# Performance work log

Hardware: AMD Instinct MI355X
Metric: run time of the kernel (lower is better)

## Reference

```python
import jax, jax.numpy as jnp
import numpy as np

B, L, IDIM = 1, 1024, 2048
H, DK, DV, K = 16, 128, 128, 4
KEY_DIM = H * DK          # 2048
VAL_DIM = H * DV          # 2048
CONV_DIM = 2 * KEY_DIM + VAL_DIM  # 6144
EPS = 1e-6


def setup_inputs() -> dict:
    key = jax.random.key(0)
    ks = jax.random.split(key, 8)
    s = 0.02
    x = jax.random.normal(ks[0], (B, L, IDIM), jnp.float32)
    Wqkv = jax.random.normal(ks[1], (IDIM, CONV_DIM), jnp.float32) * s
    Wz = jax.random.normal(ks[2], (IDIM, VAL_DIM), jnp.float32) * s
    Wb = jax.random.normal(ks[3], (IDIM, H), jnp.float32) * s
    Wa = jax.random.normal(ks[4], (IDIM, H), jnp.float32) * s
    conv_w = jax.random.normal(ks[5], (CONV_DIM, 1, K), jnp.float32) * 0.2  # depthwise [O,I/g=1,K]
    A_log = jnp.log(jax.random.uniform(ks[6], (H,), jnp.float32, 0.1, 16.0))
    dt_bias = jnp.ones((H,), jnp.float32)
    norm_w = jnp.ones((DV,), jnp.float32)
    Wout = jax.random.normal(ks[7], (VAL_DIM, IDIM), jnp.float32) * s
    return dict(x=x, Wqkv=Wqkv, Wz=Wz, Wb=Wb, Wa=Wa, conv_w=conv_w,
                A_log=A_log, dt_bias=dt_bias, norm_w=norm_w, Wout=Wout)


def _l2norm(t):
    return t * jax.lax.rsqrt(jnp.sum(t * t, axis=-1, keepdims=True) + EPS)


def reference(x, Wqkv, Wz, Wb, Wa, conv_w, A_log, dt_bias, norm_w, Wout):
    b, l, _ = x.shape
    # fused QKV projection + causal depthwise conv + SiLU
    qkv = jnp.einsum('bld,dc->blc', x, Wqkv)                 # [B,L,CONV_DIM]
    qkv = jnp.transpose(qkv, (0, 2, 1))                      # [B,C,L]
    qkv = jax.lax.conv_general_dilated(
        qkv, conv_w, window_strides=(1,), padding=[(K - 1, 0)],
        dimension_numbers=('NCL', 'OIL', 'NCL'), feature_group_count=CONV_DIM)
    qkv = jax.nn.silu(jnp.transpose(qkv, (0, 2, 1)))         # [B,L,C]
    q, k, v = jnp.split(qkv, [KEY_DIM, 2 * KEY_DIM], axis=-1)

    z = jnp.einsum('bld,dv->blv', x, Wz)                     # [B,L,VAL_DIM]
    beta = jax.nn.sigmoid(jnp.einsum('bld,dh->blh', x, Wb))  # [B,L,H]
    A = -jnp.exp(A_log)                                      # [H]
    dt = jax.nn.softplus(jnp.einsum('bld,dh->blh', x, Wa) + dt_bias)
    g = dt * A                                               # [B,L,H] (negative)

    q = _l2norm(q.reshape(b, l, H, DK))
    k = _l2norm(k.reshape(b, l, H, DK))
    v = v.reshape(b, l, H, DV)
    scale = DK ** -0.5

    # time-major for scan: [L,B,H,...]
    qs = jnp.transpose(q, (1, 0, 2, 3)) * scale
    ks_ = jnp.transpose(k, (1, 0, 2, 3))
    vs = jnp.transpose(v, (1, 0, 2, 3))
    bs = jnp.transpose(beta, (1, 0, 2))
    gs = jnp.transpose(g, (1, 0, 2))

    M0 = jnp.zeros((b, H, DK, DV), jnp.float32)

    def step(M, inp):
        q_t, k_t, v_t, b_t, g_t = inp
        M = M * jnp.exp(g_t)[..., None, None]                    # decay
        Mk = jnp.einsum('bhd,bhdv->bhv', k_t, M)                 # readout of old mem
        M = M + jnp.einsum('bhd,bhv->bhdv', k_t, (v_t - Mk) * b_t[..., None])
        o_t = jnp.einsum('bhd,bhdv->bhv', q_t, M)
        return M, o_t

    _, out = jax.lax.scan(step, M0, (qs, ks_, vs, bs, gs))   # out: [L,B,H,DV]
    out = jnp.transpose(out, (1, 0, 2, 3))                   # [B,L,H,DV]

    # RMSNormGated: rms_norm(o) * weight * silu(z)
    zg = z.reshape(b, l, H, DV)
    rms = jax.lax.rsqrt(jnp.mean(out * out, axis=-1, keepdims=True) + EPS)
    out = (out * rms) * norm_w * jax.nn.silu(zg)

    out = out.reshape(b, l, VAL_DIM)
    return jnp.einsum('blv,vd->bld', out, Wout)
```

## Files before the change

### kernel.cpp

```cpp
#include <hip/hip_runtime.h>

typedef short bf16x8 __attribute__((ext_vector_type(8)));
typedef float f32x4 __attribute__((ext_vector_type(4)));
typedef float f32x2 __attribute__((ext_vector_type(2)));
typedef unsigned short u16;
typedef u16 u16x4 __attribute__((ext_vector_type(4)));

#define L_SEQ 1024
#define IDIM_ 2048
#define H_ 16
#define DK_ 128
#define DV_ 128
#define KEYD 2048
#define VALD 2048
#define CONVD 6144
#define QZD 8320
#define GCOL 8192
#define SCH 64
#define NSC (L_SEQ / SCH)

__device__ __forceinline__ u16 f2bf(float f) {
  union { float f; unsigned u; } v; v.f = f;
  unsigned r = v.u + 0x7FFF + ((v.u >> 16) & 1);
  return (u16)(r >> 16);
}

__device__ __forceinline__ float red16(float x) {
  union U { float f; int i; } a, t;
  a.f = x;
  t.i = __builtin_amdgcn_update_dpp(0, a.i, 0xB1, 0xF, 0xF, true); a.f += t.f;
  t.i = __builtin_amdgcn_update_dpp(0, a.i, 0x4E, 0xF, 0xF, true); a.f += t.f;
  t.i = __builtin_amdgcn_update_dpp(0, a.i, 0x141, 0xF, 0xF, true); a.f += t.f;
  t.i = __builtin_amdgcn_update_dpp(0, a.i, 0x140, 0xF, 0xF, true); a.f += t.f;
  return a.f;
}

__global__ __launch_bounds__(256) void prepcast_kernel(const float* __restrict__ x,
                                                       const float* __restrict__ Wqkv,
                                                       const float* __restrict__ Wz,
                                                       const float* __restrict__ Wb,
                                                       const float* __restrict__ Wa,
                                                       const float* __restrict__ Wout,
                                                       u16* __restrict__ xb,
                                                       u16* __restrict__ WcatT,
                                                       u16* __restrict__ WoutT) {
  __shared__ float tile[32][33];
  const int bid = blockIdx.x;
  if (bid < 2048) {
    int i = (bid * 256 + threadIdx.x) * 4;
    f32x4 v = *(const f32x4*)&x[i];
    u16x4 o = { f2bf(v[0]), f2bf(v[1]), f2bf(v[2]), f2bf(v[3]) };
    *(u16x4*)&xb[i] = o;
    return;
  }
  if (bid >= 22592) {
    size_t off = (size_t)8224 * IDIM_ + (size_t)(bid - 22592) * 8192 + threadIdx.x * 32;
    u16x4 z = {0, 0, 0, 0};
#pragma unroll
    for (int j = 0; j < 8; ++j) *(u16x4*)&WcatT[off + j * 4] = z;
    return;
  }
  if (bid >= 22528) {
    int by = bid - 22528;
    int r = threadIdx.x >> 3, c8 = threadIdx.x & 7;
    int row = by * 32 + r;
#pragma unroll
    for (int cc = 0; cc < 2; ++cc) {
      int c = cc * 8 + c8;
      WcatT[(size_t)(GCOL + c) * IDIM_ + row]      = f2bf(Wb[(size_t)row * 16 + c]);
      WcatT[(size_t)(GCOL + 16 + c) * IDIM_ + row] = f2bf(Wa[(size_t)row * 16 + c]);
    }
    return;
  }
  const float* W; u16* WT; int R, C, bx, by;
  if (bid < 14336) {
    int t = bid - 2048;  bx = t % 192; by = t / 192;
    W = Wqkv; WT = WcatT; R = IDIM_; C = CONVD;
  } else if (bid < 18432) {
    int t = bid - 14336; bx = t & 63; by = t >> 6;
    W = Wz; WT = WcatT + (size_t)CONVD * IDIM_; R = IDIM_; C = VALD;
  } else {
    int t = bid - 18432; bx = t & 63; by = t >> 6;
    W = Wout; WT = WoutT; R = VALD; C = IDIM_;
  }
  int c0 = bx * 32, r0 = by * 32;
  int tx = threadIdx.x & 31, ty = threadIdx.x >> 5;
#pragma unroll
  for (int j = 0; j < 4; ++j)
    tile[ty + j * 8][tx] = W[(size_t)(r0 + ty + j * 8) * C + c0 + tx];
  __syncthreads();
#pragma unroll
  for (int j = 0; j < 4; ++j)
    WT[(size_t)(c0 + ty + j * 8) * R + r0 + tx] = f2bf(tile[tx][ty + j * 8]);
}

__global__ __launch_bounds__(256) void gemm_bt_kernel(const u16* __restrict__ A,
                                                      const u16* __restrict__ B,
                                                      float* __restrict__ C,
                                                      int M, int N, int K) {
  __shared__ short As[128 * 72];
  __shared__ short Bs[128 * 72];
  const int tid = threadIdx.x;
  const int lane = tid & 63, wave = tid >> 6;
  const int wm = wave >> 1, wn = wave & 1;
  const int m0 = blockIdx.y * 128, n0 = blockIdx.x * 128;
  const int l15 = lane & 15, lhi = lane >> 4;

  f32x4 acc[4][4] = {};

  for (int k0 = 0; k0 < K; k0 += 64) {
    __syncthreads();
#pragma unroll
    for (int i = 0; i < 4; ++i) {
      int chunk = tid + i * 256;
      int row = chunk >> 3;
      int kc = (chunk & 7) * 8;
      *(bf16x8*)&As[row * 72 + kc] =
          *(const bf16x8*)&A[(size_t)(m0 + row) * K + k0 + kc];
      *(bf16x8*)&Bs[row * 72 + kc] =
          *(const bf16x8*)&B[(size_t)(n0 + row) * K + k0 + kc];
    }
    __syncthreads();
#pragma unroll
    for (int kk = 0; kk < 64; kk += 32) {
      const int koff = kk + lhi * 8;
      bf16x8 a[4], b[4];
#pragma unroll
      for (int m = 0; m < 4; ++m)
        a[m] = *(const bf16x8*)&As[(wm * 64 + m * 16 + l15) * 72 + koff];
#pragma unroll
      for (int n = 0; n < 4; ++n)
        b[n] = *(const bf16x8*)&Bs[(wn * 64 + n * 16 + l15) * 72 + koff];
#pragma unroll
      for (int m = 0; m < 4; ++m)
#pragma unroll
        for (int n = 0; n < 4; ++n)
          acc[m][n] = __builtin_amdgcn_mfma_f32_16x16x32_bf16(a[m], b[n], acc[m][n], 0, 0, 0);
    }
  }
#pragma unroll
  for (int m = 0; m < 4; ++m)
#pragma unroll
    for (int n = 0; n < 4; ++n)
#pragma unroll
      for (int j = 0; j < 4; ++j) {
        int row = m0 + wm * 64 + m * 16 + lhi * 4 + j;
        int col = n0 + wn * 64 + n * 16 + l15;
        C[(size_t)row * N + col] = acc[m][n][j];
      }
}

__global__ __launch_bounds__(256) void gemm_bt64_kernel(const u16* __restrict__ A,
                                                        const u16* __restrict__ B,
                                                        float* __restrict__ C,
                                                        int M, int N, int K, int cxl) {
  __shared__ short As[64 * 72];
  __shared__ short Bs[128 * 72];
  const int tid = threadIdx.x;
  const int lane = tid & 63, wave = tid >> 6;
  const int wm = wave >> 1, wn = wave & 1;
  const int bid = blockIdx.x;
  const int xcd = bid & 7, bi = bid >> 3;
  const int bx = (xcd << cxl) + (bi & ((1 << cxl) - 1));
  const int by = bi >> cxl;
  const int m0 = by * 64, n0 = bx * 128;
  const int l15 = lane & 15, lhi = lane >> 4;

  f32x4 acc[2][4] = {};

  for (int k0 = 0; k0 < K; k0 += 64) {
    __syncthreads();
#pragma unroll
    for (int i = 0; i < 2; ++i) {
      int chunk = tid + i * 256;
      int row = chunk >> 3;
      int kc = (chunk & 7) * 8;
      *(bf16x8*)&As[row * 72 + kc] =
          *(const bf16x8*)&A[(size_t)(m0 + row) * K + k0 + kc];
    }
#pragma unroll
    for (int i = 0; i < 4; ++i) {
      int chunk = tid + i * 256;
      int row = chunk >> 3;
      int kc = (chunk & 7) * 8;
      *(bf16x8*)&Bs[row * 72 + kc] =
          *(const bf16x8*)&B[(size_t)(n0 + row) * K + k0 + kc];
    }
    __syncthreads();
#pragma unroll
    for (int kk = 0; kk < 64; kk += 32) {
      const int koff = kk + lhi * 8;
      bf16x8 a[2], b[4];
#pragma unroll
      for (int m = 0; m < 2; ++m)
        a[m] = *(const bf16x8*)&As[(wm * 32 + m * 16 + l15) * 72 + koff];
#pragma unroll
      for (int n = 0; n < 4; ++n)
        b[n] = *(const bf16x8*)&Bs[(wn * 64 + n * 16 + l15) * 72 + koff];
#pragma unroll
      for (int m = 0; m < 2; ++m)
#pragma unroll
        for (int n = 0; n < 4; ++n)
          acc[m][n] = __builtin_amdgcn_mfma_f32_16x16x32_bf16(a[m], b[n], acc[m][n], 0, 0, 0);
    }
  }
#pragma unroll
  for (int m = 0; m < 2; ++m)
#pragma unroll
    for (int n = 0; n < 4; ++n)
#pragma unroll
      for (int j = 0; j < 4; ++j) {
        int row = m0 + wm * 32 + m * 16 + lhi * 4 + j;
        int col = n0 + wn * 64 + n * 16 + l15;
        C[(size_t)row * N + col] = acc[m][n][j];
      }
}

__global__ __launch_bounds__(256) void gatelite_kernel(const float* __restrict__ qkvz,
                                                       const float* __restrict__ A_log,
                                                       const float* __restrict__ dt_bias,
                                                       float* __restrict__ btT,
                                                       float* __restrict__ gT) {
  int gid = blockIdx.x * 256 + threadIdx.x;
  int l = gid >> 4, h = gid & 15;
  const float* row = qkvz + (size_t)l * QZD + GCOL;
  float b = row[h], a = row[16 + h];
  btT[h * L_SEQ + l] = 1.f / (1.f + expf(-b));
  float dtv = a + dt_bias[h];
  dtv = (dtv > 20.f) ? dtv : log1pf(expf(dtv));
  gT[h * L_SEQ + l] = -expf(A_log[h]) * dtv;
}

__global__ __launch_bounds__(256) void prep2_kernel(const float* __restrict__ qkvz,
                                                    const float* __restrict__ cw,
                                                    float* __restrict__ qn,
                                                    float* __restrict__ kn,
                                                    float* __restrict__ vT) {
  __shared__ float tile[32][33];
  const int bid = blockIdx.x;
  if (bid < 4096) {
    int wid = bid * 4 + (threadIdx.x >> 6);
    int lane = threadIdx.x & 63;
    int l = wid >> 4, h = wid & 15;
    const int cq = h * 128 + lane * 2;
    const int ck = KEYD + cq;
    const float* row0 = qkvz + (size_t)l * QZD;
    f32x4 wq0 = *(const f32x4*)&cw[cq * 4];
    f32x4 wq1 = *(const f32x4*)&cw[(cq + 1) * 4];
    f32x4 wk0 = *(const f32x4*)&cw[ck * 4];
    f32x4 wk1 = *(const f32x4*)&cw[(ck + 1) * 4];
    f32x2 xq = *(const f32x2*)&row0[cq];
    f32x2 xk = *(const f32x2*)&row0[ck];
    float q0 = xq[0] * wq0[3], q1 = xq[1] * wq1[3];
    float k0 = xk[0] * wk0[3], k1 = xk[1] * wk1[3];
    if (l >= 1) {
      f32x2 aq = *(const f32x2*)&row0[cq - QZD];
      f32x2 ak = *(const f32x2*)&row0[ck - QZD];
      q0 += aq[0] * wq0[2]; q1 += aq[1] * wq1[2];
      k0 += ak[0] * wk0[2]; k1 += ak[1] * wk1[2];
    }
    if (l >= 2) {
      f32x2 aq = *(const f32x2*)&row0[cq - 2 * QZD];
      f32x2 ak = *(const f32x2*)&row0[ck - 2 * QZD];
      q0 += aq[0] * wq0[1]; q1 += aq[1] * wq1[1];
      k0 += ak[0] * wk0[1]; k1 += ak[1] * wk1[1];
    }
    if (l >= 3) {
      f32x2 aq = *(const f32x2*)&row0[cq - 3 * QZD];
      f32x2 ak = *(const f32x2*)&row0[ck - 3 * QZD];
      q0 += aq[0] * wq0[0]; q1 += aq[1] * wq1[0];
      k0 += ak[0] * wk0[0]; k1 += ak[1] * wk1[0];
    }
    f32x2 qv = { q0 / (1.f + expf(-q0)), q1 / (1.f + expf(-q1)) };
    f32x2 kv = { k0 / (1.f + expf(-k0)), k1 / (1.f + expf(-k1)) };

    float ssq = qv[0] * qv[0] + qv[1] * qv[1];
    float ssk = kv[0] * kv[0] + kv[1] * kv[1];
#pragma unroll
    for (int s = 1; s < 64; s <<= 1) {
      ssq += __shfl_xor(ssq, s);
      ssk += __shfl_xor(ssk, s);
    }
    float scq = 0.08838834764831845f / sqrtf(ssq + 1e-6f);
    float sck = 1.f / sqrtf(ssk + 1e-6f);
    qv[0] *= scq; qv[1] *= scq;
    kv[0] *= sck; kv[1] *= sck;
    size_t base = ((size_t)h * L_SEQ + l) * 128 + lane * 2;
    *(f32x2*)&qn[base] = qv;
    *(f32x2*)&kn[base] = kv;
    return;
  }
  int t = bid - 4096;
  int c0 = (t & 63) * 32, l0 = (t >> 6) * 32;
  int tx = threadIdx.x & 31, ty = threadIdx.x >> 5;
  const int c = 2 * KEYD + c0 + tx;
  f32x4 w = *(const f32x4*)&cw[c * 4];
#pragma unroll
  for (int j = 0; j < 4; ++j) {
    int l = l0 + ty + j * 8;
    const float* p = qkvz + (size_t)l * QZD + c;
    float s = p[0] * w[3];
    if (l >= 1) s += p[-QZD] * w[2];
    if (l >= 2) s += p[-2 * QZD] * w[1];
    if (l >= 3) s += p[-3 * QZD] * w[0];
    tile[ty + j * 8][tx] = s / (1.f + expf(-s));
  }
  __syncthreads();
#pragma unroll
  for (int j = 0; j < 4; ++j)
    vT[(size_t)(c0 + ty + j * 8) * L_SEQ + l0 + tx] = tile[tx][ty + j * 8];
}

__global__ __launch_bounds__(256) void winv_kernel(const float* __restrict__ kn,
                                                   const float* __restrict__ gT,
                                                   const float* __restrict__ btT,
                                                   float* __restrict__ Wg) {
  __shared__ alignas(16) u16 kb[64][136];
  __shared__ float Nl[64][65];
  __shared__ float gsh[64], Gh[64], bts[64];

  const int tid = threadIdx.x;
  const int lane = tid & 63, wave = tid >> 6;
  const int l15 = lane & 15, lhi = lane >> 4;
  const int h = blockIdx.x & 15, sc = blockIdx.x >> 4;
  const int l0 = sc * SCH;

  {
    int t = tid >> 2, c0 = (tid & 3) * 32;
    const float* kr = kn + ((size_t)h * L_SEQ + l0 + t) * 128 + c0;
#pragma unroll
    for (int j = 0; j < 8; ++j) {
      f32x4 vk = *(const f32x4*)&kr[j * 4];
      u16x4 ok = { f2bf(vk[0]), f2bf(vk[1]), f2bf(vk[2]), f2bf(vk[3]) };
      *(u16x4*)&kb[t][c0 + j * 4] = ok;
    }
  }
  if (tid < 64) {
    gsh[tid] = gT[h * L_SEQ + l0 + tid];
    bts[tid] = btT[h * L_SEQ + l0 + tid];
  }
  __syncthreads();
  if (tid < 64) {
    float a = 0.f;
    for (int u = 0; u <= tid; ++u) a += gsh[u];
    Gh[tid] = a;
  }
  __syncthreads();

  f32x4 acc1[2][2] = {};
  const int wm = wave >> 1, wn = wave & 1;
#pragma unroll
  for (int kk = 0; kk < 128; kk += 32) {
    const int koff = kk + lhi * 8;
    bf16x8 a[2], b[2];
#pragma unroll
    for (int m = 0; m < 2; ++m)
      a[m] = *(const bf16x8*)&kb[wm * 32 + m * 16 + l15][koff];
#pragma unroll
    for (int n = 0; n < 2; ++n)
      b[n] = *(const bf16x8*)&kb[wn * 32 + n * 16 + l15][koff];
#pragma unroll
    for (int m = 0; m < 2; ++m)
#pragma unroll
      for (int n = 0; n < 2; ++n)
        acc1[m][n] = __builtin_amdgcn_mfma_f32_16x16x32_bf16(a[m], b[n], acc1[m][n], 0, 0, 0);
  }
#pragma unroll
  for (int m = 0; m < 2; ++m)
#pragma unroll
    for (int n = 0; n < 2; ++n)
#pragma unroll
      for (int j = 0; j < 4; ++j) {
        int t = wm * 32 + m * 16 + lhi * 4 + j;
        int s = wn * 32 + n * 16 + l15;
        Nl[t][s] = (s < t) ? bts[t] * expf(Gh[t] - Gh[s]) * acc1[m][n][j] : 0.f;
      }
  __syncthreads();

  if (wave == 0) {
    float w[64];
    w[0] = (lane == 0) ? 1.f : 0.f;
#pragma unroll
    for (int t = 1; t < 64; ++t) {
      float a0 = (lane == t) ? 1.f : 0.f, a1 = 0.f;
#pragma unroll
      for (int s = 0; s + 1 < t; s += 2) {
        a0 = fmaf(-Nl[t][s], w[s], a0);
        a1 = fmaf(-Nl[t][s + 1], w[s + 1], a1);
      }
      if (t & 1) a0 = fmaf(-Nl[t][t - 1], w[t - 1], a0);
      w[t] = a0 + a1;
    }
    size_t base = (size_t)(sc * 16 + h) * 4096 + (size_t)lane * 64;
#pragma unroll
    for (int s = 0; s < 64; ++s) Wg[base + s] = w[s];
  }
}

__global__ __launch_bounds__(256) void wyscan_kernel(const float* __restrict__ kn,
                                                     const float* __restrict__ vT,
                                                     const float* __restrict__ gT,
                                                     const float* __restrict__ btT,
                                                     const float* __restrict__ Wg,
                                                     float* __restrict__ Mb,
                                                     float* __restrict__ DbT) {
  __shared__ alignas(16) u16 kb[64][136];
  __shared__ alignas(16) u16 kbT[128][72];
  __shared__ alignas(16) u16 Wbf[64][72];
  __shared__ alignas(16) u16 rTb[128][72];
  __shared__ alignas(16) u16 ddT[128][72];
  __shared__ alignas(16) u16 MbfT[128][136];
  __shared__ float gsh[64], Gh[64], bts[64];

  const int tid = threadIdx.x;
  const int lane = tid & 63, wave = tid >> 6;
  const int l15 = lane & 15, lhi = lane >> 4;
  const int wm = wave >> 1, wn = wave & 1;
  const int h = blockIdx.x;

  for (int i = tid; i < 128 * 136; i += 256) (&MbfT[0][0])[i] = 0;
  f32x4 Mreg[4][4];
#pragma unroll
  for (int m = 0; m < 4; ++m)
#pragma unroll
    for (int n = 0; n < 4; ++n) Mreg[m][n] = (f32x4){0.f, 0.f, 0.f, 0.f};
  __syncthreads();

#pragma unroll 1
  for (int c = 0; c < NSC; ++c) {
    const int l0 = c * SCH;
#pragma unroll
    for (int m = 0; m < 4; ++m)
#pragma unroll
      for (int n = 0; n < 4; ++n) {
        int dv = wn * 64 + n * 16 + l15;
        int dk0 = wm * 64 + m * 16 + lhi * 4;
        *(f32x4*)&Mb[(((size_t)(c * 16 + h)) * 128 + dv) * 128 + dk0] = Mreg[m][n];
      }
    {
      int t = tid >> 2, c0 = (tid & 3) * 32;
      const float* kr = kn + ((size_t)h * L_SEQ + l0 + t) * 128 + c0;
#pragma unroll
      for (int j = 0; j < 32; ++j) {
        u16 kv = f2bf(kr[j]);
        kb[t][c0 + j] = kv;
        kbT[c0 + j][t] = kv;
      }
    }
    {
      int t = tid >> 2, s0 = (tid & 3) * 16;
      size_t base = (size_t)(c * 16 + h) * 4096;
#pragma unroll
      for (int i = 0; i < 16; ++i)
        Wbf[t][s0 + i] = f2bf(Wg[base + (size_t)(s0 + i) * 64 + t]);
    }
    if (tid < 64) {
      gsh[tid] = gT[h * L_SEQ + l0 + tid];
      bts[tid] = btT[h * L_SEQ + l0 + tid];
    }
    __syncthreads();
    if (tid < 64) {
      float a = 0.f;
      for (int u = 0; u <= tid; ++u) a += gsh[u];
      Gh[tid] = a;
    }
    __syncthreads();

    {
      f32x4 acc[2][4] = {};
#pragma unroll
      for (int kk = 0; kk < 128; kk += 32) {
        const int koff = kk + lhi * 8;
        bf16x8 a[2], b[4];
#pragma unroll
        for (int m = 0; m < 2; ++m)
          a[m] = *(const bf16x8*)&kb[wm * 32 + m * 16 + l15][koff];
#pragma unroll
        for (int n = 0; n < 4; ++n)
          b[n] = *(const bf16x8*)&MbfT[wn * 64 + n * 16 + l15][koff];
#pragma unroll
        for (int m = 0; m < 2; ++m)
#pragma unroll
          for (int n = 0; n < 4; ++n)
            acc[m][n] = __builtin_amdgcn_mfma_f32_16x16x32_bf16(a[m], b[n], acc[m][n], 0, 0, 0);
      }
#pragma unroll
      for (int m = 0; m < 2; ++m)
#pragma unroll
        for (int n = 0; n < 4; ++n) {
          int dv = wn * 64 + n * 16 + l15;
          int t0 = wm * 32 + m * 16 + lhi * 4;
          f32x4 v4 = *(const f32x4*)&vT[(size_t)(h * 128 + dv) * L_SEQ + l0 + t0];
#pragma unroll
          for (int j = 0; j < 4; ++j) {
            int t = t0 + j;
            float r = bts[t] * (v4[j] - expf(Gh[t]) * acc[m][n][j]);
            rTb[dv][t] = f2bf(r);
          }
        }
    }
    __syncthreads();

    {
      f32x4 acc[2][4] = {};
#pragma unroll
      for (int kk = 0; kk < 64; kk += 32) {
        const int koff = kk + lhi * 8;
        bf16x8 a[2], b[4];
#pragma unroll
        for (int m = 0; m < 2; ++m)
          a[m] = *(const bf16x8*)&Wbf[wm * 32 + m * 16 + l15][koff];
#pragma unroll
        for (int n = 0; n < 4; ++n)
          b[n] = *(const bf16x8*)&rTb[wn * 64 + n * 16 + l15][koff];
#pragma unroll
        for (int m = 0; m < 2; ++m)
#pragma unroll
          for (int n = 0; n < 4; ++n)
            acc[m][n] = __builtin_amdgcn_mfma_f32_16x16x32_bf16(a[m], b[n], acc[m][n], 0, 0, 0);
      }
      const float G63 = Gh[63];
#pragma unroll
      for (int m = 0; m < 2; ++m)
#pragma unroll
        for (int n = 0; n < 4; ++n) {
          int dv = wn * 64 + n * 16 + l15;
          int t0 = wm * 32 + m * 16 + lhi * 4;
          *(f32x4*)&DbT[(size_t)(h * 128 + dv) * L_SEQ + l0 + t0] = acc[m][n];
#pragma unroll
          for (int j = 0; j < 4; ++j) {
            int t = t0 + j;
            ddT[dv][t] = f2bf(acc[m][n][j] * expf(G63 - Gh[t]));
          }
        }
    }
    __syncthreads();

    {
      const float E63 = expf(Gh[63]);
      f32x4 acc[4][4];
#pragma unroll
      for (int m = 0; m < 4; ++m)
#pragma unroll
        for (int n = 0; n < 4; ++n)
#pragma unroll
          for (int j = 0; j < 4; ++j) acc[m][n][j] = E63 * Mreg[m][n][j];
#pragma unroll
      for (int kk = 0; kk < 64; kk += 32) {
        const int koff = kk + lhi * 8;
        bf16x8 a[4], b[4];
#pragma unroll
        for (int m = 0; m < 4; ++m)
          a[m] = *(const bf16x8*)&kbT[wm * 64 + m * 16 + l15][koff];
#pragma unroll
        for (int n = 0; n < 4; ++n)
          b[n] = *(const bf16x8*)&ddT[wn * 64 + n * 16 + l15][koff];
#pragma unroll
        for (int m = 0; m < 4; ++m)
#pragma unroll
          for (int n = 0; n < 4; ++n)
            acc[m][n] = __builtin_amdgcn_mfma_f32_16x16x32_bf16(a[m], b[n], acc[m][n], 0, 0, 0);
      }
#pragma unroll
      for (int m = 0; m < 4; ++m)
#pragma unroll
        for (int n = 0; n < 4; ++n) {
          Mreg[m][n] = acc[m][n];
          int dv = wn * 64 + n * 16 + l15;
          int dk0 = wm * 64 + m * 16 + lhi * 4;
#pragma unroll
          for (int j = 0; j < 4; ++j)
            MbfT[dv][dk0 + j] = f2bf(acc[m][n][j]);
        }
    }
    __syncthreads();
  }
}

__global__ __launch_bounds__(256) void opass_kernel(const float* __restrict__ qn,
                                                    const float* __restrict__ kn,
                                                    const float* __restrict__ DbT,
                                                    const float* __restrict__ gT,
                                                    const float* __restrict__ Mb,
                                                    const float* __restrict__ qkvz,
                                                    const float* __restrict__ norm_w,
                                                    u16* __restrict__ gn) {
  __shared__ alignas(16) u16 qsb[64][136];
  __shared__ alignas(16) u16 bbuf[128][136];
  __shared__ alignas(16) u16 Asb[64][72];
  __shared__ float gsh[64], Gh[64];
  __shared__ float ssr[2][64];

  const int tid = threadIdx.x;
  const int lane = tid & 63, wave = tid >> 6;
  const int l15 = lane & 15, lhi = lane >> 4;
  const int h = blockIdx.x & 15, sc = blockIdx.x >> 4;
  const int l0 = sc * SCH;

  {
    int t = tid >> 2, c0 = (tid & 3) * 32;
    const float* qr = qn + ((size_t)h * L_SEQ + l0 + t) * 128 + c0;
    const float* kr = kn + ((size_t)h * L_SEQ + l0 + t) * 128 + c0;
#pragma unroll
    for (int j = 0; j < 8; ++j) {
      f32x4 vq = *(const f32x4*)&qr[j * 4];
      f32x4 vk = *(const f32x4*)&kr[j * 4];
      u16x4 oq = { f2bf(vq[0]), f2bf(vq[1]), f2bf(vq[2]), f2bf(vq[3]) };
      u16x4 ok = { f2bf(vk[0]), f2bf(vk[1]), f2bf(vk[2]), f2bf(vk[3]) };
      *(u16x4*)&qsb[t][c0 + j * 4] = oq;
      *(u16x4*)&bbuf[t][c0 + j * 4] = ok;
    }
  }
  if (tid < 64) gsh[tid] = gT[h * L_SEQ + l0 + tid];
  __syncthreads();
  if (tid < 64) {
    float a = 0.f;
    for (int u = 0; u <= tid; ++u) a += gsh[u];
    Gh[tid] = a;
  }
  __syncthreads();

  f32x4 acc1[2][2] = {};
  const int wm = wave >> 1, wn = wave & 1;
#pragma unroll
  for (int kk = 0; kk < 128; kk += 32) {
    const int koff = kk + lhi * 8;
    bf16x8 a[2], b[2];
#pragma unroll
    for (int m = 0; m < 2; ++m)
      a[m] = *(const bf16x8*)&qsb[wm * 32 + m * 16 + l15][koff];
#pragma unroll
    for (int n = 0; n < 2; ++n)
      b[n] = *(const bf16x8*)&bbuf[wn * 32 + n * 16 + l15][koff];
#pragma unroll
    for (int m = 0; m < 2; ++m)
#pragma unroll
      for (int n = 0; n < 2; ++n)
        acc1[m][n] = __builtin_amdgcn_mfma_f32_16x16x32_bf16(a[m], b[n], acc1[m][n], 0, 0, 0);
  }
#pragma unroll
  for (int m = 0; m < 2; ++m)
#pragma unroll
    for (int n = 0; n < 2; ++n)
#pragma unroll
      for (int j = 0; j < 4; ++j) {
        int t = wm * 32 + m * 16 + lhi * 4 + j;
        int s = wn * 32 + n * 16 + l15;
        float a = (s <= t) ? acc1[m][n][j] * expf(Gh[t] - Gh[s]) : 0.f;
        Asb[t][s] = f2bf(a);
      }
  __syncthreads();

  {
    int dv = tid >> 1, c0 = (tid & 1) * 64;
    const float* mr = Mb + (((size_t)sc * 16 + h) * 128 + dv) * 128 + c0;
#pragma unroll
    for (int j = 0; j < 16; ++j) {
      f32x4 v = *(const f32x4*)&mr[j * 4];
      u16x4 o = { f2bf(v[0]), f2bf(v[1]), f2bf(v[2]), f2bf(v[3]) };
      *(u16x4*)&bbuf[dv][c0 + j * 4] = o;
    }
  }
  __syncthreads();

  f32x4 acc[2][4] = {};
#pragma unroll
  for (int kk = 0; kk < 128; kk += 32) {
    const int koff = kk + lhi * 8;
    bf16x8 a[2], b[4];
#pragma unroll
    for (int m = 0; m < 2; ++m)
      a[m] = *(const bf16x8*)&qsb[wm * 32 + m * 16 + l15][koff];
#pragma unroll
    for (int n = 0; n < 4; ++n)
      b[n] = *(const bf16x8*)&bbuf[wn * 64 + n * 16 + l15][koff];
#pragma unroll
    for (int m = 0; m < 2; ++m)
#pragma unroll
      for (int n = 0; n < 4; ++n)
        acc[m][n] = __builtin_amdgcn_mfma_f32_16x16x32_bf16(a[m], b[n], acc[m][n], 0, 0, 0);
  }
#pragma unroll
  for (int m = 0; m < 2; ++m) {
#pragma unroll
    for (int j = 0; j < 4; ++j) {
      int t = wm * 32 + m * 16 + lhi * 4 + j;
      float sc1 = expf(Gh[t]);
#pragma unroll
      for (int n = 0; n < 4; ++n) acc[m][n][j] *= sc1;
    }
  }
  __syncthreads();

  {
    int dv = tid >> 1, c0 = (tid & 1) * 32;
    const float* dr = DbT + (size_t)(h * 128 + dv) * L_SEQ + l0 + c0;
#pragma unroll
    for (int j = 0; j < 8; ++j) {
      f32x4 v = *(const f32x4*)&dr[j * 4];
      u16x4 o = { f2bf(v[0]), f2bf(v[1]), f2bf(v[2]), f2bf(v[3]) };
      *(u16x4*)&bbuf[dv][c0 + j * 4] = o;
    }
  }
  __syncthreads();

#pragma unroll
  for (int kk = 0; kk < 64; kk += 32) {
    const int koff = kk + lhi * 8;
    bf16x8 a[2], b[4];
#pragma unroll
    for (int m = 0; m < 2; ++m)
      a[m] = *(const bf16x8*)&Asb[wm * 32 + m * 16 + l15][koff];
#pragma unroll
    for (int n = 0; n < 4; ++n)
      b[n] = *(const bf16x8*)&bbuf[wn * 64 + n * 16 + l15][koff];
#pragma unroll
    for (int m = 0; m < 2; ++m)
#pragma unroll
      for (int n = 0; n < 4; ++n)
        acc[m][n] = __builtin_amdgcn_mfma_f32_16x16x32_bf16(a[m], b[n], acc[m][n], 0, 0, 0);
  }

  float pr[2][4];
#pragma unroll
  for (int m = 0; m < 2; ++m)
#pragma unroll
    for (int j = 0; j < 4; ++j) {
      float p = 0.f;
#pragma unroll
      for (int n = 0; n < 4; ++n) p = fmaf(acc[m][n][j], acc[m][n][j], p);
      pr[m][j] = red16(p);
    }
  if (l15 == 0) {
#pragma unroll
    for (int m = 0; m < 2; ++m)
#pragma unroll
      for (int j = 0; j < 4; ++j)
        ssr[wn][wm * 32 + m * 16 + lhi * 4 + j] = pr[m][j];
  }
  __syncthreads();
#pragma unroll
  for (int m = 0; m < 2; ++m)
#pragma unroll
    for (int j = 0; j < 4; ++j) {
      int t = wm * 32 + m * 16 + lhi * 4 + j;
      float ss = ssr[0][t] + ssr[1][t];
      float r = 1.f / sqrtf(ss * (1.f / 128.f) + 1e-6f);
      const float* zp = qkvz + (size_t)(l0 + t) * QZD + CONVD + h * 128;
      u16* dst = gn + (size_t)(l0 + t) * VALD + h * 128;
#pragma unroll
      for (int n = 0; n < 4; ++n) {
        int dv = wn * 64 + n * 16 + l15;
        float z = zp[dv];
        float sil = z / (1.f + expf(-z));
        dst[dv] = f2bf(acc[m][n][j] * r * norm_w[dv] * sil);
      }
    }
}

extern "C" void kernel_launch(void* const* d_in, const int* in_sizes, int n_in,
                              void* d_out, int out_size, void* d_ws, size_t ws_size,
                              hipStream_t stream) {
  const float* x      = (const float*)d_in[0];
  const float* Wqkv   = (const float*)d_in[1];
  const float* Wz     = (const float*)d_in[2];
  const float* Wb     = (const float*)d_in[3];
  const float* Wa     = (const float*)d_in[4];
  const float* conv_w = (const float*)d_in[5];
  const float* A_log  = (const float*)d_in[6];
  const float* dt_bias= (const float*)d_in[7];
  const float* norm_w = (const float*)d_in[8];
  const float* Wout   = (const float*)d_in[9];
  float* out = (float*)d_out;

  char* ws = (char*)d_ws;
  size_t off = 0;
  auto alloc = [&](size_t bytes) {
    void* p = ws + off;
    off = (off + bytes + 255) & ~(size_t)255;
    return p;
  };
  u16* xb     = (u16*)alloc((size_t)L_SEQ * IDIM_ * 2);
  u16* WcatT  = (u16*)alloc((size_t)QZD * IDIM_ * 2);
  u16* WoutT  = (u16*)alloc((size_t)IDIM_ * VALD * 2);
  float* qkvz = (float*)alloc((size_t)L_SEQ * QZD * 4);
  float* qn   = (float*)alloc((size_t)H_ * L_SEQ * 128 * 4);
  float* kn   = (float*)alloc((size_t)H_ * L_SEQ * 128 * 4);
  float* vT   = (float*)alloc((size_t)H_ * 128 * L_SEQ * 4);
  float* btT  = (float*)alloc((size_t)L_SEQ * H_ * 4);
  float* gTb  = (float*)alloc((size_t)L_SEQ * H_ * 4);
  float* Wgb  = (float*)alloc((size_t)NSC * H_ * 64 * 64 * 4);
  float* Mb   = (float*)alloc((size_t)NSC * H_ * 128 * 128 * 4);
  float* DbT  = (float*)alloc((size_t)H_ * 128 * L_SEQ * 4);
  u16* gn     = (u16*)alloc((size_t)L_SEQ * VALD * 2);

  prepcast_kernel<<<22616, 256, 0, stream>>>(x, Wqkv, Wz, Wb, Wa, Wout, xb, WcatT, WoutT);

  gemm_bt_kernel<<<dim3(QZD / 128, L_SEQ / 128), 256, 0, stream>>>(xb, WcatT, qkvz, L_SEQ, QZD, IDIM_);

  gatelite_kernel<<<64, 256, 0, stream>>>(qkvz, A_log, dt_bias, btT, gTb);

  prep2_kernel<<<6144, 256, 0, stream>>>(qkvz, conv_w, qn, kn, vT);

  winv_kernel<<<NSC * H_, 256, 0, stream>>>(kn, gTb, btT, Wgb);
  wyscan_kernel<<<H_, 256, 0, stream>>>(kn, vT, gTb, btT, Wgb, Mb, DbT);

  opass_kernel<<<NSC * H_, 256, 0, stream>>>(qn, kn, DbT, gTb, Mb, qkvz, norm_w, gn);

  gemm_bt64_kernel<<<256, 256, 0, stream>>>(gn, WoutT, out, L_SEQ, IDIM_, VALD, 1);
}
```

Before: 362.8 us.

## Split wyscan state across DV slabs to launch four blocks per head

The sequential chunked state-update kernel now splits the 128-wide value dimension into four 32-wide slabs, so it launches 64 blocks instead of 16. Each block carries a quarter of the state matrix in registers and shared memory, which shortens the serial per-chunk chain and uses more compute units. In exchange every slab block redundantly loads and converts the key chunk and W matrix. The global loads of k and W are also vectorised to float4, and a barrier is added after the state store.

```diff
diff --git a/kernel.cpp b/kernel.cpp
--- a/kernel.cpp
+++ b/kernel.cpp
@@ -407,52 +407,61 @@
   __shared__ alignas(16) u16 kb[64][136];
   __shared__ alignas(16) u16 kbT[128][72];
   __shared__ alignas(16) u16 Wbf[64][72];
-  __shared__ alignas(16) u16 rTb[128][72];
-  __shared__ alignas(16) u16 ddT[128][72];
-  __shared__ alignas(16) u16 MbfT[128][136];
+  __shared__ alignas(16) u16 rTb[32][72];
+  __shared__ alignas(16) u16 ddT[32][72];
+  __shared__ alignas(16) u16 MbfT[32][136];
   __shared__ float gsh[64], Gh[64], bts[64];
 
   const int tid = threadIdx.x;
   const int lane = tid & 63, wave = tid >> 6;
   const int l15 = lane & 15, lhi = lane >> 4;
   const int wm = wave >> 1, wn = wave & 1;
-  const int h = blockIdx.x;
-
-  for (int i = tid; i < 128 * 136; i += 256) (&MbfT[0][0])[i] = 0;
-  f32x4 Mreg[4][4];
-#pragma unroll
-  for (int m = 0; m < 4; ++m)
-#pragma unroll
-    for (int n = 0; n < 4; ++n) Mreg[m][n] = (f32x4){0.f, 0.f, 0.f, 0.f};
+  const int h = blockIdx.x & 15, slab = blockIdx.x >> 4;
+  const int dv0 = slab * 32;
+  const int dvl = wn * 16 + l15;
+
+  for (int i = tid; i < 32 * 136; i += 256) (&MbfT[0][0])[i] = 0;
+  f32x4 Mreg[4];
+#pragma unroll
+  for (int m = 0; m < 4; ++m) Mreg[m] = (f32x4){0.f, 0.f, 0.f, 0.f};
   __syncthreads();
 
 #pragma unroll 1
   for (int c = 0; c < NSC; ++c) {
     const int l0 = c * SCH;
 #pragma unroll
-    for (int m = 0; m < 4; ++m)
-#pragma unroll
-      for (int n = 0; n < 4; ++n) {
-        int dv = wn * 64 + n * 16 + l15;
-        int dk0 = wm * 64 + m * 16 + lhi * 4;
-        *(f32x4*)&Mb[(((size_t)(c * 16 + h)) * 128 + dv) * 128 + dk0] = Mreg[m][n];
-      }
+    for (int m = 0; m < 4; ++m) {
+      int dk0 = wm * 64 + m * 16 + lhi * 4;
+      *(f32x4*)&Mb[(((size_t)(c * 16 + h)) * 128 + dv0 + dvl) * 128 + dk0] = Mreg[m];
+    }
+    __syncthreads();
+
     {
       int t = tid >> 2, c0 = (tid & 3) * 32;
       const float* kr = kn + ((size_t)h * L_SEQ + l0 + t) * 128 + c0;
 #pragma unroll
-      for (int j = 0; j < 32; ++j) {
-        u16 kv = f2bf(kr[j]);
-        kb[t][c0 + j] = kv;
-        kbT[c0 + j][t] = kv;
+      for (int j4 = 0; j4 < 8; ++j4) {
+        f32x4 v = *(const f32x4*)&kr[j4 * 4];
+        u16x4 o = { f2bf(v[0]), f2bf(v[1]), f2bf(v[2]), f2bf(v[3]) };
+        *(u16x4*)&kb[t][c0 + j4 * 4] = o;
+        kbT[c0 + j4 * 4 + 0][t] = o[0];
+        kbT[c0 + j4 * 4 + 1][t] = o[1];
+        kbT[c0 + j4 * 4 + 2][t] = o[2];
+        kbT[c0 + j4 * 4 + 3][t] = o[3];
       }
     }
     {
-      int t = tid >> 2, s0 = (tid & 3) * 16;
       size_t base = (size_t)(c * 16 + h) * 4096;
 #pragma unroll
-      for (int i = 0; i < 16; ++i)
-        Wbf[t][s0 + i] = f2bf(Wg[base + (size_t)(s0 + i) * 64 + t]);
+      for (int i = 0; i < 4; ++i) {
+        int flat = tid + i * 256;
+        int s = flat >> 4, t0 = (flat & 15) * 4;
+        f32x4 v = *(const f32x4*)&Wg[base + (size_t)s * 64 + t0];
+        Wbf[t0 + 0][s] = f2bf(v[0]);
+        Wbf[t0 + 1][s] = f2bf(v[1]);
+        Wbf[t0 + 2][s] = f2bf(v[2]);
+        Wbf[t0 + 3][s] = f2bf(v[3]);
+      }
     }
     if (tid < 64) {
       gsh[tid] = gT[h * L_SEQ + l0 + tid];
@@ -467,111 +476,82 @@
     __syncthreads();
 
     {
-      f32x4 acc[2][4] = {};
+      f32x4 acc[2] = {};
 #pragma unroll
       for (int kk = 0; kk < 128; kk += 32) {
         const int koff = kk + lhi * 8;
-        bf16x8 a[2], b[4];
-#pragma unroll
-        for (int m = 0; m < 2; ++m)
-          a[m] = *(const bf16x8*)&kb[wm * 32 + m * 16 + l15][koff];
-#pragma unroll
-        for (int n = 0; n < 4; ++n)
-          b[n] = *(const bf16x8*)&MbfT[wn * 64 + n * 16 + l15][koff];
-#pragma unroll
-        for (int m = 0; m < 2; ++m)
-#pragma unroll
-          for (int n = 0; n < 4; ++n)
-            acc[m][n] = __builtin_amdgcn_mfma_f32_16x16x32_bf16(a[m], b[n], acc[m][n], 0, 0, 0);
-      }
-#pragma unroll
-      for (int m = 0; m < 2; ++m)
-#pragma unroll
-        for (int n = 0; n < 4; ++n) {
-          int dv = wn * 64 + n * 16 + l15;
-          int t0 = wm * 32 + m * 16 + lhi * 4;
-          f32x4 v4 = *(const f32x4*)&vT[(size_t)(h * 128 + dv) * L_SEQ + l0 + t0];
-#pragma unroll
-          for (int j = 0; j < 4; ++j) {
-            int t = t0 + j;
-            float r = bts[t] * (v4[j] - expf(Gh[t]) * acc[m][n][j]);
-            rTb[dv][t] = f2bf(r);
-          }
+        bf16x8 b0 = *(const bf16x8*)&MbfT[dvl][koff];
+#pragma unroll
+        for (int m = 0; m < 2; ++m) {
+          bf16x8 a = *(const bf16x8*)&kb[wm * 32 + m * 16 + l15][koff];
+          acc[m] = __builtin_amdgcn_mfma_f32_16x16x32_bf16(a, b0, acc[m], 0, 0, 0);
         }
+      }
+#pragma unroll
+      for (int m = 0; m < 2; ++m) {
+        int t0 = wm * 32 + m * 16 + lhi * 4;
+        f32x4 v4 = *(const f32x4*)&vT[(size_t)(h * 128 + dv0 + dvl) * L_SEQ + l0 + t0];
+#pragma unroll
+        for (int j = 0; j < 4; ++j) {
+          int t = t0 + j;
+          float r = bts[t] * (v4[j] - expf(Gh[t]) * acc[m][j]);
+          rTb[dvl][t] = f2bf(r);
+        }
+      }
     }
     __syncthreads();
 
     {
-      f32x4 acc[2][4] = {};
+      f32x4 acc[2] = {};
 #pragma unroll
       for (int kk = 0; kk < 64; kk += 32) {
         const int koff = kk + lhi * 8;
-        bf16x8 a[2], b[4];
-#pragma unroll
-        for (int m = 0; m < 2; ++m)
-          a[m] = *(const bf16x8*)&Wbf[wm * 32 + m * 16 + l15][koff];
-#pragma unroll
-        for (int n = 0; n < 4; ++n)
-          b[n] = *(const bf16x8*)&rTb[wn * 64 + n * 16 + l15][koff];
-#pragma unroll
-        for (int m = 0; m < 2; ++m)
-#pragma unroll
-          for (int n = 0; n < 4; ++n)
-            acc[m][n] = __builtin_amdgcn_mfma_f32_16x16x32_bf16(a[m], b[n], acc[m][n], 0, 0, 0);
+        bf16x8 b0 = *(const bf16x8*)&rTb[dvl][koff];
+#pragma unroll
+        for (int m = 0; m < 2; ++m) {
+          bf16x8 a = *(const bf16x8*)&Wbf[wm * 32 + m * 16 + l15][koff];
+          acc[m] = __builtin_amdgcn_mfma_f32_16x16x32_bf16(a, b0, acc[m], 0, 0, 0);
+        }
       }
       const float G63 = Gh[63];
 #pragma unroll
-      for (int m = 0; m < 2; ++m)
-#pragma unroll
-        for (int n = 0; n < 4; ++n) {
-          int dv = wn * 64 + n * 16 + l15;
-          int t0 = wm * 32 + m * 16 + lhi * 4;
-          *(f32x4*)&DbT[(size_t)(h * 128 + dv) * L_SEQ + l0 + t0] = acc[m][n];
-#pragma unroll
-          for (int j = 0; j < 4; ++j) {
-            int t = t0 + j;
-            ddT[dv][t] = f2bf(acc[m][n][j] * expf(G63 - Gh[t]));
-          }
+      for (int m = 0; m < 2; ++m) {
+        int t0 = wm * 32 + m * 16 + lhi * 4;
+        *(f32x4*)&DbT[(size_t)(h * 128 + dv0 + dvl) * L_SEQ + l0 + t0] = acc[m];
+#pragma unroll
+        for (int j = 0; j < 4; ++j) {
+          int t = t0 + j;
+          ddT[dvl][t] = f2bf(acc[m][j] * expf(G63 - Gh[t]));
         }
+      }
     }
     __syncthreads();
 
     {
       const float E63 = expf(Gh[63]);
-      f32x4 acc[4][4];
+      f32x4 acc[4];
 #pragma unroll
       for (int m = 0; m < 4; ++m)
 #pragma unroll
-        for (int n = 0; n < 4; ++n)
-#pragma unroll
-          for (int j = 0; j < 4; ++j) acc[m][n][j] = E63 * Mreg[m][n][j];
+        for (int j = 0; j < 4; ++j) acc[m][j] = E63 * Mreg[m][j];
 #pragma unroll
       for (int kk = 0; kk < 64; kk += 32) {
         const int koff = kk + lhi * 8;
-        bf16x8 a[4], b[4];
-#pragma unroll
-        for (int m = 0; m < 4; ++m)
-          a[m] = *(const bf16x8*)&kbT[wm * 64 + m * 16 + l15][koff];
-#pragma unroll
-        for (int n = 0; n < 4; ++n)
-          b[n] = *(const bf16x8*)&ddT[wn * 64 + n * 16 + l15][koff];
-#pragma unroll
-        for (int m = 0; m < 4; ++m)
-#pragma unroll
-          for (int n = 0; n < 4; ++n)
-            acc[m][n] = __builtin_amdgcn_mfma_f32_16x16x32_bf16(a[m], b[n], acc[m][n], 0, 0, 0);
-      }
-#pragma unroll
-      for (int m = 0; m < 4; ++m)
-#pragma unroll
-        for (int n = 0; n < 4; ++n) {
-          Mreg[m][n] = acc[m][n];
-          int dv = wn * 64 + n * 16 + l15;
-          int dk0 = wm * 64 + m * 16 + lhi * 4;
-#pragma unroll
-          for (int j = 0; j < 4; ++j)
-            MbfT[dv][dk0 + j] = f2bf(acc[m][n][j]);
+        bf16x8 b0 = *(const bf16x8*)&ddT[dvl][koff];
+#pragma unroll
+        for (int m = 0; m < 4; ++m) {
+          bf16x8 a = *(const bf16x8*)&kbT[wm * 64 + m * 16 + l15][koff];
+          acc[m] = __builtin_amdgcn_mfma_f32_16x16x32_bf16(a, b0, acc[m], 0, 0, 0);
         }
+      }
+#pragma unroll
+      for (int m = 0; m < 4; ++m) {
+        Mreg[m] = acc[m];
+        int dk0 = wm * 64 + m * 16 + lhi * 4;
+#pragma unroll
+        for (int j = 0; j < 4; ++j)
+          MbfT[dvl][dk0 + j] = f2bf(acc[m][j]);
+      }
     }
     __syncthreads();
   }
@@ -803,7 +783,7 @@
   prep2_kernel<<<6144, 256, 0, stream>>>(qkvz, conv_w, qn, kn, vT);
 
   winv_kernel<<<NSC * H_, 256, 0, stream>>>(kn, gTb, btT, Wgb);
-  wyscan_kernel<<<H_, 256, 0, stream>>>(kn, vT, gTb, btT, Wgb, Mb, DbT);
+  wyscan_kernel<<<H_ * 4, 256, 0, stream>>>(kn, vT, gTb, btT, Wgb, Mb, DbT);
 
   opass_kernel<<<NSC * H_, 256, 0, stream>>>(qn, kn, DbT, gTb, Mb, qkvz, norm_w, gn);
 
```

Measured after the change: 305.7 us. -15.7%, faster.
